# Optimization experiments

Measured on AMD Instinct MI355X. Metric: run time of the kernel, lower is better.

## Reference

```python
import jax, jax.numpy as jnp
import numpy as np

DIM = 512
NUM_HEADS = 1
WS = 16
B, H, W = 2, WS * WS, 1


def _rel_pos_index(ws):
    # matches Attention.calculate_relative_position_index (no Swin offset -> negatives)
    coords = np.stack(np.meshgrid(np.arange(ws), np.arange(ws), indexing='ij'), 0).reshape(2, -1)
    rel = coords[:, :, None] - coords[:, None, :]          # [2, ws^2, ws^2]
    return rel.transpose(1, 2, 0).sum(-1)                  # [ws^2, ws^2] in [-(2ws-2), 2ws-2]

_NTAB = (2 * WS - 1) ** 2
# torch fancy indexing wraps negative indices; emulate with mod (values are in (-NTAB, NTAB))
_RPI = np.mod(_rel_pos_index(WS), _NTAB).reshape(-1)       # [ws^4]


def setup_inputs() -> dict:
    key = jax.random.key(0)
    ks = jax.random.split(key, 6)
    x = jax.random.normal(ks[0], (B, DIM, H, W), dtype=jnp.float32)
    qkv_w = jax.random.normal(ks[1], (3 * DIM, DIM), dtype=jnp.float32) * (DIM ** -0.5)
    qkv_b = jax.random.normal(ks[2], (3 * DIM,), dtype=jnp.float32) * 0.02
    proj_w = jax.random.normal(ks[3], (DIM, DIM), dtype=jnp.float32) * (DIM ** -0.5)
    proj_b = jax.random.normal(ks[4], (DIM,), dtype=jnp.float32) * 0.02
    rpb = jax.random.normal(ks[5], (_NTAB, NUM_HEADS), dtype=jnp.float32) * 0.02
    return {"x": x, "qkv_w": qkv_w, "qkv_b": qkv_b,
            "proj_w": proj_w, "proj_b": proj_b, "rpb": rpb}


def reference(x, qkv_w, qkv_b, proj_w, proj_b, rpb):
    b, c, h, w = x.shape                                   # [B, C, H, W=1]
    d = c // NUM_HEADS
    scale = d ** -0.5                                      # qk_scale=None -> (dim//nh)^-0.5
    # 1x1 conv == channel matmul
    qkv = jnp.einsum('bchw,oc->bohw', x, qkv_w) + qkv_b[None, :, None, None]
    qkv = qkv.reshape(b, 3, NUM_HEADS, d, h, w)
    q, k, v = qkv[:, 0], qkv[:, 1], qkv[:, 2]              # [B, nh, d, H, W]
    # matmul over last two dims: contracts W -> [B, nh, d, H, H]
    attn = jnp.einsum('bndhw,bndgw->bndhg', q, k) * scale
    idx = jnp.asarray(_RPI)
    bias = rpb[idx].reshape(h * w, h * w, -1).transpose(2, 0, 1)  # [nh, HW, HW] = [1, H, H]
    attn = jax.nn.softmax(attn + bias, axis=-1)
    out = jnp.einsum('bndhg,bndgw->bndhw', attn, v).sum(axis=1)   # sum over heads -> [B, d, H, W]
    out = jnp.einsum('bchw,oc->bohw', out, proj_w) + proj_b[None, :, None, None]
    return out
```

## Files before the change

### kernel.cpp

```cpp
#include <hip/hip_runtime.h>
#include <hip/hip_bf16.h>


#define TOK   256
#define KDIM  512
#define LOG2E 1.4426950408889634f
#define SCALE 0.04419417382415922f
#define NPART 8
#define QPSTRIDE 786432
#define PPSTRIDE 262144

#define EXP2(x) __builtin_amdgcn_exp2f(x)

template<int BM, int KSPLIT>
__global__ __launch_bounds__(256)
void gemm_f32(const float* __restrict__ A, const float* __restrict__ B,
              float* __restrict__ C, int M)
{
    constexpr int KLEN  = KDIM / KSPLIT;
    constexpr int NITER = KLEN / 16;
    constexpr int MM    = BM / 16;
    constexpr int LDA   = BM + 4;

    __shared__ float As[2][16][LDA];
    __shared__ float Bs[2][16][64];

    const int t  = threadIdx.x;
    const int o0 = blockIdx.x * BM;
    const int n0 = blockIdx.y * 64;
    const int b  = blockIdx.z & 1;
    const int ks = blockIdx.z >> 1;

    const float* Ab = A + (size_t)o0 * KDIM + ks * KLEN;
    const float* Bb = B + ((size_t)b * KDIM + (size_t)ks * KLEN) * TOK + n0;
    float*       Cb = C + ((size_t)blockIdx.z * M + o0) * TOK + n0;

    const int ar  = t >> 2;
    const int ac4 = (t & 3) * 4;
    const int bk  = t >> 4;
    const int bn4 = (t & 15) * 4;

    float4 ra0, ra1, rb;
#define LOAD_TILE(IT) do {                                                   \
        const int k0_ = (IT) * 16;                                           \
        ra0 = *(const float4*)(Ab + (size_t)ar * KDIM + k0_ + ac4);          \
        if (BM == 128)                                                       \
            ra1 = *(const float4*)(Ab + (size_t)(64 + ar) * KDIM + k0_ + ac4);\
        rb  = *(const float4*)(Bb + (size_t)(k0_ + bk) * TOK + bn4);         \
    } while (0)
#define STORE_TILE(BUF) do {                                                 \
        As[BUF][ac4 + 0][ar] = ra0.x;                                        \
        As[BUF][ac4 + 1][ar] = ra0.y;                                        \
        As[BUF][ac4 + 2][ar] = ra0.z;                                        \
        As[BUF][ac4 + 3][ar] = ra0.w;                                        \
        if (BM == 128) {                                                     \
            As[BUF][ac4 + 0][64 + ar] = ra1.x;                               \
            As[BUF][ac4 + 1][64 + ar] = ra1.y;                               \
            As[BUF][ac4 + 2][64 + ar] = ra1.z;                               \
            As[BUF][ac4 + 3][64 + ar] = ra1.w;                               \
        }                                                                    \
        *(float4*)&Bs[BUF][bk][bn4] = rb;                                    \
    } while (0)

    const int m0 = (t >> 4) * MM;
    const int n4 = (t & 15) * 4;

    float acc[MM][4];
#pragma unroll
    for (int i = 0; i < MM; ++i)
#pragma unroll
        for (int j = 0; j < 4; ++j) acc[i][j] = 0.f;

    LOAD_TILE(0);
    STORE_TILE(0);
    if (NITER > 1) LOAD_TILE(1);
    __syncthreads();

#pragma unroll
    for (int it = 0; it < NITER; ++it) {
        const int cur = it & 1;
        if (it + 1 < NITER) STORE_TILE(1 - cur);
        if (it + 2 < NITER) LOAD_TILE(it + 2);
#pragma unroll
        for (int kk = 0; kk < 16; ++kk) {
            const float4 b4 = *(const float4*)&Bs[cur][kk][n4];
            float af[MM];
#pragma unroll
            for (int mi = 0; mi < MM; mi += 4) {
                const float4 a4 = *(const float4*)&As[cur][kk][m0 + mi];
                af[mi + 0] = a4.x; af[mi + 1] = a4.y;
                af[mi + 2] = a4.z; af[mi + 3] = a4.w;
            }
#pragma unroll
            for (int mi = 0; mi < MM; ++mi) {
                acc[mi][0] = fmaf(af[mi], b4.x, acc[mi][0]);
                acc[mi][1] = fmaf(af[mi], b4.y, acc[mi][1]);
                acc[mi][2] = fmaf(af[mi], b4.z, acc[mi][2]);
                acc[mi][3] = fmaf(af[mi], b4.w, acc[mi][3]);
            }
        }
        __syncthreads();
    }

#pragma unroll
    for (int mi = 0; mi < MM; ++mi) {
        const float4 o4 = make_float4(acc[mi][0], acc[mi][1], acc[mi][2], acc[mi][3]);
        *(float4*)(Cb + (size_t)(m0 + mi) * TOK + n4) = o4;
    }
#undef LOAD_TILE
#undef STORE_TILE
}

__global__ __launch_bounds__(256)
void attn_f32(const float* __restrict__ qkvp, const float* __restrict__ qkv_b,
              const float* __restrict__ rpb, float* __restrict__ aout)
{
    __shared__ float ks_[2][TOK];
    __shared__ float vs_[2][TOK];
    __shared__ float tab2[64];
    __shared__ float brow[31][258];
    __shared__ float lpart[2][TOK];
    __shared__ float apart[2][TOK];

    const int t  = threadIdx.x;
    const int b  = blockIdx.y;
    const int d0 = blockIdx.x * 2;
    const float* q0 = qkvp + (size_t)b * (1536 * TOK);

    if (t < 61) {
        const int rel = t - 30;
        tab2[t] = rpb[rel < 0 ? rel + 961 : rel] * LOG2E;
    }
    {
        const int sel = t >> 7;
        const int row = (t >> 6) & 1;
        const int g4  = (t & 63) * 4;
        const int o   = (sel ? 1024 : 512) + d0 + row;
        const float* p = q0 + (size_t)o * TOK + g4;
        const float bb = qkv_b[o];
        float4 v = make_float4(bb, bb, bb, bb);
#pragma unroll
        for (int pp = 0; pp < NPART; ++pp) {
            const float4 x = *(const float4*)(p + (size_t)pp * QPSTRIDE);
            v.x += x.x; v.y += x.y; v.z += x.z; v.w += x.w;
        }
        if (sel == 0) {
            const float s = SCALE * LOG2E;
            v.x *= s; v.y *= s; v.z *= s; v.w *= s;
            *(float4*)&ks_[row][g4] = v;
        } else {
            *(float4*)&vs_[row][g4] = v;
        }
    }
    __syncthreads();
    {
        const int rg = ((t >> 4) & 15) + (t & 15);
#pragma unroll 1
        for (int it = 0; it < 31; ++it)
            brow[it][t] = tab2[it - rg + 30];
    }
    __syncthreads();

    const int w   = t >> 6;
    const int dl  = w & 1;
    const int gh  = w >> 1;
    const int hl  = t & 63;
    const int qi  = ((hl & 15) << 2) | (hl >> 4);
    const int h0  = qi * 4;
    const int rh0 = (qi >> 2) + 4 * (qi & 3);

    float q[4];
    {
        const float* p = q0 + (size_t)(d0 + dl) * TOK + h0;
        const float bb = qkv_b[d0 + dl];
        q[0] = bb; q[1] = bb; q[2] = bb; q[3] = bb;
#pragma unroll
        for (int pp = 0; pp < NPART; ++pp) {
            const float4 x = *(const float4*)(p + (size_t)pp * QPSTRIDE);
            q[0] += x.x; q[1] += x.y; q[2] += x.z; q[3] += x.w;
        }
    }

    float l[4]  = {0.f, 0.f, 0.f, 0.f};
    float am[4] = {0.f, 0.f, 0.f, 0.f};

    const int pbeg = gh * 128;
#pragma unroll 2
    for (int p = pbeg; p < pbeg + 128; p += 4) {
        const float4 k4 = *(const float4*)&ks_[dl][p];
        const float4 v4 = *(const float4*)&vs_[dl][p];
#pragma unroll
        for (int r = 0; r < 4; ++r) {
            const float2 b01 = *(const float2*)&brow[rh0 + r][p];
            const float2 b23 = *(const float2*)&brow[rh0 + r][p + 2];
            float e;
            e = EXP2(fmaf(q[r], k4.x, b01.x)); l[r] += e; am[r] = fmaf(e, v4.x, am[r]);
            e = EXP2(fmaf(q[r], k4.y, b01.y)); l[r] += e; am[r] = fmaf(e, v4.y, am[r]);
            e = EXP2(fmaf(q[r], k4.z, b23.x)); l[r] += e; am[r] = fmaf(e, v4.z, am[r]);
            e = EXP2(fmaf(q[r], k4.w, b23.y)); l[r] += e; am[r] = fmaf(e, v4.w, am[r]);
        }
    }

    if (gh == 1) {
        *(float4*)&lpart[dl][h0] = make_float4(l[0], l[1], l[2], l[3]);
        *(float4*)&apart[dl][h0] = make_float4(am[0], am[1], am[2], am[3]);
    }
    __syncthreads();
    if (gh == 0) {
        const float4 lo = *(const float4*)&lpart[dl][h0];
        const float4 ao = *(const float4*)&apart[dl][h0];
        float4 o4;
        o4.x = (am[0] + ao.x) / (l[0] + lo.x);
        o4.y = (am[1] + ao.y) / (l[1] + lo.y);
        o4.z = (am[2] + ao.z) / (l[2] + lo.z);
        o4.w = (am[3] + ao.w) / (l[3] + lo.w);
        *(float4*)(aout + ((size_t)b * 512 + d0 + dl) * TOK + h0) = o4;
    }
}

__global__ __launch_bounds__(256)
void combine_f32(const float* __restrict__ pp, const float* __restrict__ pb,
                 float* __restrict__ out)
{
    const int gid  = blockIdx.x * 256 + threadIdx.x;
    const int flat = gid * 4;
    const int o = (flat >> 8) & 511;
    float4 a = make_float4(pb[o], pb[o], pb[o], pb[o]);
#pragma unroll
    for (int p = 0; p < NPART; ++p) {
        const float4 x = *(const float4*)(pp + (size_t)p * PPSTRIDE + flat);
        a.x += x.x; a.y += x.y; a.z += x.z; a.w += x.w;
    }
    *(float4*)(out + flat) = a;
}

extern "C" void kernel_launch(void* const* d_in, const int* in_sizes, int n_in,
                              void* d_out, int out_size, void* d_ws, size_t ws_size,
                              hipStream_t stream)
{
    const float* x      = (const float*)d_in[0];
    const float* qkv_w  = (const float*)d_in[1];
    const float* qkv_b  = (const float*)d_in[2];
    const float* proj_w = (const float*)d_in[3];
    const float* proj_b = (const float*)d_in[4];
    const float* rpb    = (const float*)d_in[5];
    float* out = (float*)d_out;
    float* ws  = (float*)d_ws;

    float* qkvp  = ws;
    float* aout  = ws + 6291456;
    float* projp = ws + 6553600;

    gemm_f32<128, 8><<<dim3(12, 4, 16), 256, 0, stream>>>(qkv_w, x, qkvp, 1536);

    attn_f32<<<dim3(256, 2), 256, 0, stream>>>(qkvp, qkv_b, rpb, aout);

    gemm_f32<64, 8><<<dim3(8, 4, 16), 256, 0, stream>>>(proj_w, aout, projp, 512);

    combine_f32<<<dim3(256), 256, 0, stream>>>(projp, proj_b, out);
}
```

Before: 103.3 us.

## Fuse all four stages into one persistent kernel with grid-wide atomic barriers

Replaces the four separate launches (QKV GEMM, attention, projection GEMM, split-K combine) with a single 512-block kernel. The stages are separated by software grid barriers built from atomic counters, and a memset before the launch resets those counters. The stages share one union of shared-memory buffers. The QKV GEMM tile grows to 192 rows so the work maps onto exactly 512 blocks. The goal is to remove the launch gaps between kernels, at the risk of deadlock if not all 512 blocks are resident at once, plus the cost of barrier spinning and an extra memset launch.

Result: slower. 260.8 us (+152.4%).

```diff
diff --git a/kernel.cpp b/kernel.cpp
--- a/kernel.cpp
+++ b/kernel.cpp
@@ -9,61 +9,73 @@
 #define NPART 8
 #define QPSTRIDE 786432
 #define PPSTRIDE 262144
+#define NBLK  512
 
 #define EXP2(x) __builtin_amdgcn_exp2f(x)
 
-template<int BM, int KSPLIT>
-__global__ __launch_bounds__(256)
-void gemm_f32(const float* __restrict__ A, const float* __restrict__ B,
-              float* __restrict__ C, int M)
-{
-    constexpr int KLEN  = KDIM / KSPLIT;
+union Smem {
+    struct { float As[2][16][196]; float Bs[2][16][64]; } g1;
+    struct { float As[2][16][68];  float Bs[2][16][64]; } g3;
+    struct {
+        float ks_[2][TOK], vs_[2][TOK];
+        float tab2[64];
+        float brow[31][258];
+        float lpart[2][TOK], apart[2][TOK];
+    } at;
+};
+
+__device__ __forceinline__ void gbar(int* cnt)
+{
+    __syncthreads();
+    if (threadIdx.x == 0) {
+        __threadfence();
+        __hip_atomic_fetch_add(cnt, 1, __ATOMIC_RELAXED, __HIP_MEMORY_SCOPE_AGENT);
+        while (__hip_atomic_fetch_add(cnt, 0, __ATOMIC_RELAXED,
+                                      __HIP_MEMORY_SCOPE_AGENT) < NBLK)
+            __builtin_amdgcn_s_sleep(2);
+        __threadfence();
+    }
+    __syncthreads();
+}
+
+template<int BM, int KLEN>
+__device__ __forceinline__ void gemm_dev(const float* __restrict__ Ab,
+                                         const float* __restrict__ Bb,
+                                         float* __restrict__ Cb,
+                                         float* sA, float* sB)
+{
     constexpr int NITER = KLEN / 16;
     constexpr int MM    = BM / 16;
+    constexpr int SEG   = BM / 64;
     constexpr int LDA   = BM + 4;
 
-    __shared__ float As[2][16][LDA];
-    __shared__ float Bs[2][16][64];
-
-    const int t  = threadIdx.x;
-    const int o0 = blockIdx.x * BM;
-    const int n0 = blockIdx.y * 64;
-    const int b  = blockIdx.z & 1;
-    const int ks = blockIdx.z >> 1;
-
-    const float* Ab = A + (size_t)o0 * KDIM + ks * KLEN;
-    const float* Bb = B + ((size_t)b * KDIM + (size_t)ks * KLEN) * TOK + n0;
-    float*       Cb = C + ((size_t)blockIdx.z * M + o0) * TOK + n0;
-
+    const int t   = threadIdx.x;
     const int ar  = t >> 2;
     const int ac4 = (t & 3) * 4;
     const int bk  = t >> 4;
     const int bn4 = (t & 15) * 4;
-
-    float4 ra0, ra1, rb;
-#define LOAD_TILE(IT) do {                                                   \
-        const int k0_ = (IT) * 16;                                           \
-        ra0 = *(const float4*)(Ab + (size_t)ar * KDIM + k0_ + ac4);          \
-        if (BM == 128)                                                       \
-            ra1 = *(const float4*)(Ab + (size_t)(64 + ar) * KDIM + k0_ + ac4);\
-        rb  = *(const float4*)(Bb + (size_t)(k0_ + bk) * TOK + bn4);         \
-    } while (0)
-#define STORE_TILE(BUF) do {                                                 \
-        As[BUF][ac4 + 0][ar] = ra0.x;                                        \
-        As[BUF][ac4 + 1][ar] = ra0.y;                                        \
-        As[BUF][ac4 + 2][ar] = ra0.z;                                        \
-        As[BUF][ac4 + 3][ar] = ra0.w;                                        \
-        if (BM == 128) {                                                     \
-            As[BUF][ac4 + 0][64 + ar] = ra1.x;                               \
-            As[BUF][ac4 + 1][64 + ar] = ra1.y;                               \
-            As[BUF][ac4 + 2][64 + ar] = ra1.z;                               \
-            As[BUF][ac4 + 3][64 + ar] = ra1.w;                               \
-        }                                                                    \
-        *(float4*)&Bs[BUF][bk][bn4] = rb;                                    \
-    } while (0)
-
-    const int m0 = (t >> 4) * MM;
-    const int n4 = (t & 15) * 4;
+    const int m0  = (t >> 4) * MM;
+    const int n4  = (t & 15) * 4;
+
+    float4 ra[SEG], rb;
+    auto LOAD = [&](int it) {
+        const int k0 = it * 16;
+#pragma unroll
+        for (int s = 0; s < SEG; ++s)
+            ra[s] = *(const float4*)(Ab + (size_t)(s * 64 + ar) * KDIM + k0 + ac4);
+        rb = *(const float4*)(Bb + (size_t)(k0 + bk) * TOK + bn4);
+    };
+    auto STORE = [&](int buf) {
+        float* As = sA + buf * 16 * LDA;
+#pragma unroll
+        for (int s = 0; s < SEG; ++s) {
+            As[(ac4 + 0) * LDA + s * 64 + ar] = ra[s].x;
+            As[(ac4 + 1) * LDA + s * 64 + ar] = ra[s].y;
+            As[(ac4 + 2) * LDA + s * 64 + ar] = ra[s].z;
+            As[(ac4 + 3) * LDA + s * 64 + ar] = ra[s].w;
+        }
+        *(float4*)(sB + buf * 16 * 64 + bk * 64 + bn4) = rb;
+    };
 
     float acc[MM][4];
 #pragma unroll
@@ -71,23 +83,24 @@
 #pragma unroll
         for (int j = 0; j < 4; ++j) acc[i][j] = 0.f;
 
-    LOAD_TILE(0);
-    STORE_TILE(0);
-    if (NITER > 1) LOAD_TILE(1);
+    LOAD(0); STORE(0);
+    if (NITER > 1) LOAD(1);
     __syncthreads();
 
 #pragma unroll
     for (int it = 0; it < NITER; ++it) {
         const int cur = it & 1;
-        if (it + 1 < NITER) STORE_TILE(1 - cur);
-        if (it + 2 < NITER) LOAD_TILE(it + 2);
+        if (it + 1 < NITER) STORE(1 - cur);
+        if (it + 2 < NITER) LOAD(it + 2);
+        const float* As = sA + cur * 16 * LDA;
+        const float* Bs = sB + cur * 16 * 64;
 #pragma unroll
         for (int kk = 0; kk < 16; ++kk) {
-            const float4 b4 = *(const float4*)&Bs[cur][kk][n4];
+            const float4 b4 = *(const float4*)(Bs + kk * 64 + n4);
             float af[MM];
 #pragma unroll
             for (int mi = 0; mi < MM; mi += 4) {
-                const float4 a4 = *(const float4*)&As[cur][kk][m0 + mi];
+                const float4 a4 = *(const float4*)(As + kk * LDA + m0 + mi);
                 af[mi + 0] = a4.x; af[mi + 1] = a4.y;
                 af[mi + 2] = a4.z; af[mi + 3] = a4.w;
             }
@@ -103,135 +116,154 @@
     }
 
 #pragma unroll
-    for (int mi = 0; mi < MM; ++mi) {
-        const float4 o4 = make_float4(acc[mi][0], acc[mi][1], acc[mi][2], acc[mi][3]);
-        *(float4*)(Cb + (size_t)(m0 + mi) * TOK + n4) = o4;
-    }
-#undef LOAD_TILE
-#undef STORE_TILE
-}
-
-__global__ __launch_bounds__(256)
-void attn_f32(const float* __restrict__ qkvp, const float* __restrict__ qkv_b,
-              const float* __restrict__ rpb, float* __restrict__ aout)
-{
-    __shared__ float ks_[2][TOK];
-    __shared__ float vs_[2][TOK];
-    __shared__ float tab2[64];
-    __shared__ float brow[31][258];
-    __shared__ float lpart[2][TOK];
-    __shared__ float apart[2][TOK];
-
-    const int t  = threadIdx.x;
-    const int b  = blockIdx.y;
-    const int d0 = blockIdx.x * 2;
-    const float* q0 = qkvp + (size_t)b * (1536 * TOK);
-
-    if (t < 61) {
-        const int rel = t - 30;
-        tab2[t] = rpb[rel < 0 ? rel + 961 : rel] * LOG2E;
-    }
-    {
-        const int sel = t >> 7;
-        const int row = (t >> 6) & 1;
-        const int g4  = (t & 63) * 4;
-        const int o   = (sel ? 1024 : 512) + d0 + row;
-        const float* p = q0 + (size_t)o * TOK + g4;
-        const float bb = qkv_b[o];
-        float4 v = make_float4(bb, bb, bb, bb);
-#pragma unroll
-        for (int pp = 0; pp < NPART; ++pp) {
-            const float4 x = *(const float4*)(p + (size_t)pp * QPSTRIDE);
-            v.x += x.x; v.y += x.y; v.z += x.z; v.w += x.w;
-        }
-        if (sel == 0) {
-            const float s = SCALE * LOG2E;
-            v.x *= s; v.y *= s; v.z *= s; v.w *= s;
-            *(float4*)&ks_[row][g4] = v;
-        } else {
-            *(float4*)&vs_[row][g4] = v;
-        }
-    }
-    __syncthreads();
-    {
-        const int rg = ((t >> 4) & 15) + (t & 15);
+    for (int mi = 0; mi < MM; ++mi)
+        *(float4*)(Cb + (size_t)(m0 + mi) * TOK + n4) =
+            make_float4(acc[mi][0], acc[mi][1], acc[mi][2], acc[mi][3]);
+}
+
+__global__ __launch_bounds__(256, 2)
+void fused_attn(const float* __restrict__ x, const float* __restrict__ qkv_w,
+                const float* __restrict__ qkv_b, const float* __restrict__ proj_w,
+                const float* __restrict__ proj_b, const float* __restrict__ rpb,
+                float* __restrict__ out, float* __restrict__ ws)
+{
+    __shared__ Smem sm;
+    const int blk = blockIdx.x;
+    const int t   = threadIdx.x;
+
+    int*   bar   = (int*)ws;
+    float* qkvp  = ws + 64;
+    float* aoutp = qkvp + 6291456;
+    float* projp = aoutp + 262144;
+
+    {
+        const int nt = blk & 3, mt = (blk >> 2) & 7, z = blk >> 5;
+        const int b = z & 1, ks = z >> 1;
+        gemm_dev<192, 64>(qkv_w + (size_t)(mt * 192) * KDIM + ks * 64,
+                          x + ((size_t)b * KDIM + ks * 64) * TOK + nt * 64,
+                          qkvp + ((size_t)z * 1536 + mt * 192) * TOK + nt * 64,
+                          &sm.g1.As[0][0][0], &sm.g1.Bs[0][0][0]);
+    }
+    gbar(bar + 0);
+
+    {
+        const int b  = blk >> 8;
+        const int d0 = (blk & 255) * 2;
+        const float* q0 = qkvp + (size_t)b * (1536 * TOK);
+
+        if (t < 61) {
+            const int rel = t - 30;
+            sm.at.tab2[t] = rpb[rel < 0 ? rel + 961 : rel] * LOG2E;
+        }
+        {
+            const int sel = t >> 7;
+            const int row = (t >> 6) & 1;
+            const int g4  = (t & 63) * 4;
+            const int o   = (sel ? 1024 : 512) + d0 + row;
+            const float* p = q0 + (size_t)o * TOK + g4;
+            const float bb = qkv_b[o];
+            float4 v = make_float4(bb, bb, bb, bb);
+#pragma unroll
+            for (int pp = 0; pp < NPART; ++pp) {
+                const float4 xv = *(const float4*)(p + (size_t)pp * QPSTRIDE);
+                v.x += xv.x; v.y += xv.y; v.z += xv.z; v.w += xv.w;
+            }
+            if (sel == 0) {
+                const float s = SCALE * LOG2E;
+                v.x *= s; v.y *= s; v.z *= s; v.w *= s;
+                *(float4*)&sm.at.ks_[row][g4] = v;
+            } else {
+                *(float4*)&sm.at.vs_[row][g4] = v;
+            }
+        }
+        __syncthreads();
+        {
+            const int rg = ((t >> 4) & 15) + (t & 15);
 #pragma unroll 1
-        for (int it = 0; it < 31; ++it)
-            brow[it][t] = tab2[it - rg + 30];
-    }
-    __syncthreads();
-
-    const int w   = t >> 6;
-    const int dl  = w & 1;
-    const int gh  = w >> 1;
-    const int hl  = t & 63;
-    const int qi  = ((hl & 15) << 2) | (hl >> 4);
-    const int h0  = qi * 4;
-    const int rh0 = (qi >> 2) + 4 * (qi & 3);
-
-    float q[4];
-    {
-        const float* p = q0 + (size_t)(d0 + dl) * TOK + h0;
-        const float bb = qkv_b[d0 + dl];
-        q[0] = bb; q[1] = bb; q[2] = bb; q[3] = bb;
-#pragma unroll
-        for (int pp = 0; pp < NPART; ++pp) {
-            const float4 x = *(const float4*)(p + (size_t)pp * QPSTRIDE);
-            q[0] += x.x; q[1] += x.y; q[2] += x.z; q[3] += x.w;
-        }
-    }
-
-    float l[4]  = {0.f, 0.f, 0.f, 0.f};
-    float am[4] = {0.f, 0.f, 0.f, 0.f};
-
-    const int pbeg = gh * 128;
+            for (int it = 0; it < 31; ++it)
+                sm.at.brow[it][t] = sm.at.tab2[it - rg + 30];
+        }
+        __syncthreads();
+
+        const int w   = t >> 6;
+        const int dl  = w & 1;
+        const int gh  = w >> 1;
+        const int hl  = t & 63;
+        const int qi  = ((hl & 15) << 2) | (hl >> 4);
+        const int h0  = qi * 4;
+        const int rh0 = (qi >> 2) + 4 * (qi & 3);
+
+        float q[4];
+        {
+            const float* p = q0 + (size_t)(d0 + dl) * TOK + h0;
+            const float bb = qkv_b[d0 + dl];
+            q[0] = bb; q[1] = bb; q[2] = bb; q[3] = bb;
+#pragma unroll
+            for (int pp = 0; pp < NPART; ++pp) {
+                const float4 xv = *(const float4*)(p + (size_t)pp * QPSTRIDE);
+                q[0] += xv.x; q[1] += xv.y; q[2] += xv.z; q[3] += xv.w;
+            }
+        }
+
+        float l[4]  = {0.f, 0.f, 0.f, 0.f};
+        float am[4] = {0.f, 0.f, 0.f, 0.f};
+        const int pbeg = gh * 128;
 #pragma unroll 2
-    for (int p = pbeg; p < pbeg + 128; p += 4) {
-        const float4 k4 = *(const float4*)&ks_[dl][p];
-        const float4 v4 = *(const float4*)&vs_[dl][p];
-#pragma unroll
-        for (int r = 0; r < 4; ++r) {
-            const float2 b01 = *(const float2*)&brow[rh0 + r][p];
-            const float2 b23 = *(const float2*)&brow[rh0 + r][p + 2];
-            float e;
-            e = EXP2(fmaf(q[r], k4.x, b01.x)); l[r] += e; am[r] = fmaf(e, v4.x, am[r]);
-            e = EXP2(fmaf(q[r], k4.y, b01.y)); l[r] += e; am[r] = fmaf(e, v4.y, am[r]);
-            e = EXP2(fmaf(q[r], k4.z, b23.x)); l[r] += e; am[r] = fmaf(e, v4.z, am[r]);
-            e = EXP2(fmaf(q[r], k4.w, b23.y)); l[r] += e; am[r] = fmaf(e, v4.w, am[r]);
-        }
-    }
-
-    if (gh == 1) {
-        *(float4*)&lpart[dl][h0] = make_float4(l[0], l[1], l[2], l[3]);
-        *(float4*)&apart[dl][h0] = make_float4(am[0], am[1], am[2], am[3]);
-    }
-    __syncthreads();
-    if (gh == 0) {
-        const float4 lo = *(const float4*)&lpart[dl][h0];
-        const float4 ao = *(const float4*)&apart[dl][h0];
-        float4 o4;
-        o4.x = (am[0] + ao.x) / (l[0] + lo.x);
-        o4.y = (am[1] + ao.y) / (l[1] + lo.y);
-        o4.z = (am[2] + ao.z) / (l[2] + lo.z);
-        o4.w = (am[3] + ao.w) / (l[3] + lo.w);
-        *(float4*)(aout + ((size_t)b * 512 + d0 + dl) * TOK + h0) = o4;
-    }
-}
-
-__global__ __launch_bounds__(256)
-void combine_f32(const float* __restrict__ pp, const float* __restrict__ pb,
-                 float* __restrict__ out)
-{
-    const int gid  = blockIdx.x * 256 + threadIdx.x;
-    const int flat = gid * 4;
-    const int o = (flat >> 8) & 511;
-    float4 a = make_float4(pb[o], pb[o], pb[o], pb[o]);
-#pragma unroll
-    for (int p = 0; p < NPART; ++p) {
-        const float4 x = *(const float4*)(pp + (size_t)p * PPSTRIDE + flat);
-        a.x += x.x; a.y += x.y; a.z += x.z; a.w += x.w;
-    }
-    *(float4*)(out + flat) = a;
+        for (int p = pbeg; p < pbeg + 128; p += 4) {
+            const float4 k4 = *(const float4*)&sm.at.ks_[dl][p];
+            const float4 v4 = *(const float4*)&sm.at.vs_[dl][p];
+#pragma unroll
+            for (int r = 0; r < 4; ++r) {
+                const float2 b01 = *(const float2*)&sm.at.brow[rh0 + r][p];
+                const float2 b23 = *(const float2*)&sm.at.brow[rh0 + r][p + 2];
+                float e;
+                e = EXP2(fmaf(q[r], k4.x, b01.x)); l[r] += e; am[r] = fmaf(e, v4.x, am[r]);
+                e = EXP2(fmaf(q[r], k4.y, b01.y)); l[r] += e; am[r] = fmaf(e, v4.y, am[r]);
+                e = EXP2(fmaf(q[r], k4.z, b23.x)); l[r] += e; am[r] = fmaf(e, v4.z, am[r]);
+                e = EXP2(fmaf(q[r], k4.w, b23.y)); l[r] += e; am[r] = fmaf(e, v4.w, am[r]);
+            }
+        }
+
+        if (gh == 1) {
+            *(float4*)&sm.at.lpart[dl][h0] = make_float4(l[0], l[1], l[2], l[3]);
+            *(float4*)&sm.at.apart[dl][h0] = make_float4(am[0], am[1], am[2], am[3]);
+        }
+        __syncthreads();
+        if (gh == 0) {
+            const float4 lo = *(const float4*)&sm.at.lpart[dl][h0];
+            const float4 ao = *(const float4*)&sm.at.apart[dl][h0];
+            float4 o4;
+            o4.x = (am[0] + ao.x) / (l[0] + lo.x);
+            o4.y = (am[1] + ao.y) / (l[1] + lo.y);
+            o4.z = (am[2] + ao.z) / (l[2] + lo.z);
+            o4.w = (am[3] + ao.w) / (l[3] + lo.w);
+            *(float4*)(aoutp + ((size_t)b * 512 + d0 + dl) * TOK + h0) = o4;
+        }
+    }
+    gbar(bar + 1);
+
+    {
+        const int nt = blk & 3, mt = (blk >> 2) & 7, z = blk >> 5;
+        const int b = z & 1, ks = z >> 1;
+        gemm_dev<64, 64>(proj_w + (size_t)(mt * 64) * KDIM + ks * 64,
+                         aoutp + ((size_t)b * KDIM + ks * 64) * TOK + nt * 64,
+                         projp + ((size_t)z * 512 + mt * 64) * TOK + nt * 64,
+                         &sm.g3.As[0][0][0], &sm.g3.Bs[0][0][0]);
+    }
+    gbar(bar + 2);
+
+    {
+        const int flat2 = (blk * 256 + t) * 2;
+        const int o = (flat2 >> 8) & 511;
+        const float bb = proj_b[o];
+        float2 a = make_float2(bb, bb);
+#pragma unroll
+        for (int p = 0; p < NPART; ++p) {
+            const float2 xv = *(const float2*)(projp + (size_t)p * PPSTRIDE + flat2);
+            a.x += xv.x; a.y += xv.y;
+        }
+        *(float2*)(out + flat2) = a;
+    }
 }
 
 extern "C" void kernel_launch(void* const* d_in, const int* in_sizes, int n_in,
@@ -247,15 +279,8 @@
     float* out = (float*)d_out;
     float* ws  = (float*)d_ws;
 
-    float* qkvp  = ws;
-    float* aout  = ws + 6291456;
-    float* projp = ws + 6553600;
-
-    gemm_f32<128, 8><<<dim3(12, 4, 16), 256, 0, stream>>>(qkv_w, x, qkvp, 1536);
-
-    attn_f32<<<dim3(256, 2), 256, 0, stream>>>(qkvp, qkv_b, rpb, aout);
-
-    gemm_f32<64, 8><<<dim3(8, 4, 16), 256, 0, stream>>>(proj_w, aout, projp, 512);
-
-    combine_f32<<<dim3(256), 256, 0, stream>>>(projp, proj_b, out);
-}
+    hipMemsetAsync(d_ws, 0, 256, stream);
+
+    fused_attn<<<dim3(NBLK), 256, 0, stream>>>(x, qkv_w, qkv_b, proj_w, proj_b,
+                                               rpb, out, ws);
+}
```
